# Performance work log

Measured on AMD Instinct MI355X. Metric: run time of the kernel, lower is better.

## Reference

```python
import jax, jax.numpy as jnp
import numpy as np
from jax import lax

N_C = 1024  # number of FPS centroids (hard-coded in forward)
K = 32      # knn neighbors (hard-coded in forward)


def _fps(x, far0):
    # Faithful to the source: dist is recomputed against ONLY the latest
    # centroid each iteration (the mask/min-update in the source is dead code),
    # then far = argmax(dist).
    B = x.shape[0]
    bidx = jnp.arange(B)

    def step(far, _):
        c = x[bidx, far]                              # [B, C]
        d = jnp.sum((x - c[:, None, :]) ** 2, -1)     # [B, N]
        return jnp.argmax(d, -1), c

    _, cents = lax.scan(step, far0, None, length=N_C)  # cents: [n_c, B, C]
    return jnp.transpose(cents, (1, 0, 2))             # [B, n_c, C]


def _knn_group(x, cent):
    # squared euclidean distances (same argsort order as torch.cdist)
    d2 = (jnp.sum(cent ** 2, -1)[..., None]
          + jnp.sum(x ** 2, -1)[:, None, :]
          - 2.0 * jnp.einsum('bmc,bnc->bmn', cent, x))   # [B, n_c, N]
    _, idx = lax.top_k(-d2, K)                            # [B, n_c, K] smallest dists
    neighbors = jax.vmap(lambda xb, ib: xb[ib])(x, idx)   # [B, n_c, K, C]
    return neighbors


def _conv1x1(h, w, b):
    # 1x1 Conv1d == channel matmul; h: [B, Cin, L], w: [Cout, Cin]
    return jax.nn.relu(jnp.einsum('oi,bil->bol', w, h) + b[None, :, None])


def setup_inputs() -> dict:
    key = jax.random.key(0)
    ks = jax.random.split(key, 20)
    B, N, C = 4, 16384, 3
    num_classes = 3
    p = lambda k, shp: (jax.random.normal(k, shp, jnp.float32) * 0.02)
    return {
        'x': jax.random.normal(ks[0], (B, N, C), jnp.float32),
        'far_init': jax.random.randint(ks[1], (B,), 0, N, jnp.int32),
        'w1': p(ks[2], (64, 3)),    'b1': p(ks[3], (64,)),
        'w2': p(ks[4], (64, 64)),   'b2': p(ks[5], (64,)),
        'w3': p(ks[6], (64, 64)),   'b3': p(ks[7], (64,)),
        'w4': p(ks[8], (128, 64)),  'b4': p(ks[9], (128,)),
        'w5': p(ks[10], (1024, 128)), 'b5': p(ks[11], (1024,)),
        'fw1': p(ks[12], (512, 1024)), 'fb1': p(ks[13], (512,)),
        'fw2': p(ks[14], (256, 512)),  'fb2': p(ks[15], (256,)),
        'fw3': p(ks[16], (num_classes, 256)), 'fb3': p(ks[17], (num_classes,)),
    }


def reference(x, far_init, w1, b1, w2, b2, w3, b3, w4, b4, w5, b5,
              fw1, fb1, fw2, fb2, fw3, fb3):
    B, N, C = x.shape
    cent = _fps(x, far_init)                 # [B, n_c, C]
    neighbors = _knn_group(x, cent)          # [B, n_c, K, C]
    h = jnp.transpose(neighbors, (0, 3, 1, 2)).reshape(B, C, N_C * K)
    h = _conv1x1(h, w1, b1)
    h = _conv1x1(h, w2, b2)
    h = _conv1x1(h, w3, b3)
    h = _conv1x1(h, w4, b4)
    h = _conv1x1(h, w5, b5)                  # [B, 1024, n_c*K]
    g = jnp.max(h, axis=2)                   # global max pool -> [B, 1024]
    g = jax.nn.relu(g @ fw1.T + fb1)
    g = jax.nn.relu(g @ fw2.T + fb2)
    return g @ fw3.T + fb3                   # [B, num_classes]
```

## Files before the change

kernel.cpp:

```cpp
#include <hip/hip_runtime.h>

#define BN  4
#define NPT 16384
#define NCC 1024
#define KNN 32

#define HBINS    2048
#define CCH      4
#define CAND_CAP 768

#define OFF_CCOUNT 0
#define OFF_SCOUNT 64
#define OFF_SBITS  128
#define OFF_POOL   (128 + BN*(NPT/32)*4)
#define OFF_CLIST  (OFF_POOL + BN*NCC*4)
#define OFF_H1     (OFF_CLIST + BN*NCC*4)
#define OFF_SLIST  (OFF_H1 + BN*512*4)

typedef short bf16x8 __attribute__((ext_vector_type(8)));
typedef float f32x4  __attribute__((ext_vector_type(4)));
typedef float f32x2  __attribute__((ext_vector_type(2)));

__device__ __forceinline__ short f2bf(float f) {
    unsigned u = __float_as_uint(f);
    return (short)((u + 0x7fffu + ((u >> 16) & 1u)) >> 16);
}
__device__ __forceinline__ bf16x8 cvt8(const float* __restrict__ p) {
    bf16x8 v;
#pragma unroll
    for (int j = 0; j < 8; ++j) v[j] = f2bf(p[j]);
    return v;
}

__global__ __launch_bounds__(512) void fps_kernel(const float* __restrict__ x,
    const int* __restrict__ far_init, int* __restrict__ clist, int* __restrict__ ccount,
    int* __restrict__ scount, unsigned* __restrict__ sbits, float* __restrict__ pool)
{
#pragma clang fp contract(off)
    const int b = blockIdx.x, t = threadIdx.x;
    __shared__ __align__(16) unsigned char seen[NPT];
    __shared__ unsigned long long slot[3];

    sbits[b*(NPT/32) + t] = 0u;
    pool[b*NCC + t] = 0.0f;
    pool[b*NCC + 512 + t] = 0.0f;
    if (t == 0) { ccount[b] = 0; scount[b] = 0; }

    const float* xb = x + (size_t)b * NPT * 3;
    f32x2 px[16], py[16], pz[16];
#pragma unroll
    for (int q = 0; q < 16; ++q) {
        int ia = t + (q << 10), ib = ia + 512;
        px[q] = f32x2{xb[ia*3+0], xb[ib*3+0]};
        py[q] = f32x2{xb[ia*3+1], xb[ib*3+1]};
        pz[q] = f32x2{xb[ia*3+2], xb[ib*3+2]};
    }
    ((uint4*)seen)[t]       = make_uint4(0,0,0,0);
    ((uint4*)seen)[t + 512] = make_uint4(0,0,0,0);
    if (t == 0) { slot[0] = 0ull; slot[1] = 0ull; slot[2] = 0ull; }
    int prev_bx = far_init[b];
    __syncthreads();
    int pbs = __builtin_amdgcn_readfirstlane(prev_bx);
    float cx = xb[pbs*3], cy = xb[pbs*3+1], cz = xb[pbs*3+2];

    int done = 0;
    for (int it = 0; it < NCC-1; ++it) {
        const int p = it % 3;
        const f32x2 cX = {cx, cx}, cY = {cy, cy}, cZ = {cz, cz};
        float best = -1.0f; int bi = 0;
#pragma unroll
        for (int q = 0; q < 16; ++q) {
            f32x2 dx = px[q] - cX;
            f32x2 dy = py[q] - cY;
            f32x2 dz = pz[q] - cZ;
            f32x2 m1 = dx * dx;
            f32x2 m2 = dy * dy;
            f32x2 m3 = dz * dz;
            f32x2 s  = (m1 + m2) + m3;
            int ia = t + (q << 10);
            if (s.x > best) { best = s.x; bi = ia; }
            if (s.y > best) { best = s.y; bi = ia + 512; }
        }
#pragma unroll
        for (int m = 1; m < 64; m <<= 1) {
            float od = __shfl_xor(best, m, 64);
            int   oi = __shfl_xor(bi,   m, 64);
            if (od > best || (od == best && oi < bi)) { best = od; bi = oi; }
        }
        if ((t & 63) == 0) {
            unsigned long long pk =
                (((unsigned long long)__float_as_uint(best)) << 32)
                | (unsigned)(NPT - 1 - bi);
            atomicMax(&slot[p], pk);
        }
        if (t == 0) seen[prev_bx] = 1;
        __syncthreads();
        int bx = NPT - 1 - (int)(unsigned)(slot[p] & 0xFFFFFFFFull);
        if (t == 0) slot[(it + 2) % 3] = 0ull;
        if (seen[bx]) { done = 1; break; }
        prev_bx = bx;
        int bxs = __builtin_amdgcn_readfirstlane(bx);
        cx = xb[bxs*3]; cy = xb[bxs*3+1]; cz = xb[bxs*3+2];
    }
    if (!done && t == 0) seen[prev_bx] = 1;
    __syncthreads();
#pragma unroll
    for (int j = 0; j < 32; ++j) {
        int idx = t + (j << 9);
        if (seen[idx]) {
            int pos = atomicAdd(&ccount[b], 1);
            clist[b * NCC + pos] = idx;
        }
    }
}

__device__ __forceinline__ unsigned key_of(float px, float py, float pz, float xn,
                                           float cx, float cy, float cz, float cn)
{
    float dot = __fadd_rn(__fadd_rn(__fmul_rn(cx,px), __fmul_rn(cy,py)), __fmul_rn(cz,pz));
    float d2  = __fsub_rn(__fadd_rn(cn, xn), __fmul_rn(2.0f, dot));
    unsigned u = __float_as_uint(d2);
    return u ^ ((u >> 31) ? 0xFFFFFFFFu : 0x80000000u);
}

__device__ __forceinline__ void wave_scan_bins(const unsigned* __restrict__ H,
    int nbins, int rem, int lane, int* __restrict__ out_bin, int* __restrict__ out_below)
{
    int per = nbins >> 6;
    int base = lane * per;
    unsigned part = 0;
    for (int q = 0; q < per; ++q) part += H[base + q];
    unsigned inc = part;
#pragma unroll
    for (int m = 1; m < 64; m <<= 1) {
        unsigned u = __shfl_up(inc, m, 64);
        if (lane >= m) inc += u;
    }
    unsigned exc = inc - part;
    unsigned long long mk = __ballot(exc < (unsigned)rem && inc >= (unsigned)rem);
    int src = __ffsll((long long)mk) - 1;
    if (lane == src) {
        unsigned run = exc; int bb = base;
        for (int q = 0; q < per; ++q) {
            unsigned h = H[base + q];
            if (run + h >= (unsigned)rem) { bb = base + q; break; }
            run += h;
        }
        *out_bin = bb; *out_below = (int)run;
    }
}

__global__ __launch_bounds__(1024) void knn_kernel(const float* __restrict__ x,
    const int* __restrict__ clist, const int* __restrict__ ccount,
    unsigned* __restrict__ sbits, int* __restrict__ slist, int* __restrict__ scount)
{
    const int b = blockIdx.y, t = threadIdx.x;
    const int lane = t & 63, w = t >> 6;
    const int cnt = ccount[b];
    const int cbase = blockIdx.x * CCH;
    if (cbase >= cnt) return;
    const float* xb = x + (size_t)b * NPT * 3;

    __shared__ unsigned hist[CCH * HBINS];
    __shared__ unsigned cand[CCH * CAND_CAP];
    __shared__ float cpx[CCH], cpy[CCH], cpz[CCH], cpn[CCH];
    __shared__ unsigned candCnt[CCH];
    __shared__ int s_bb[CCH], s_below[CCH], s_rrem[CCH], s_need[CCH], s_pref[CCH];
    __shared__ unsigned s_tau[CCH];
    __shared__ int s_tbin, s_tbelow;

    if (t < CCH) {
        int ci = clist[b * NCC + min(cbase + t, cnt - 1)];
        float cx = xb[ci*3], cy = xb[ci*3+1], cz = xb[ci*3+2];
        cpx[t] = cx; cpy[t] = cy; cpz[t] = cz;
        cpn[t] = __fadd_rn(__fadd_rn(__fmul_rn(cx,cx), __fmul_rn(cy,cy)), __fmul_rn(cz,cz));
        candCnt[t] = 0;
    }
    for (int i = t; i < CCH * HBINS; i += 1024) hist[i] = 0;
    __syncthreads();

    for (int j = 0; j < NPT/1024; ++j) {
        int i = t + (j << 10);
        float px = xb[i*3], py = xb[i*3+1], pz = xb[i*3+2];
        float xn = __fadd_rn(__fadd_rn(__fmul_rn(px,px), __fmul_rn(py,py)), __fmul_rn(pz,pz));
#pragma unroll
        for (int c = 0; c < CCH; ++c) {
            unsigned key = key_of(px,py,pz,xn, cpx[c],cpy[c],cpz[c],cpn[c]);
            atomicAdd(&hist[c*HBINS + (key >> 21)], 1u);
        }
    }
    __syncthreads();

    if (w < CCH)
        wave_scan_bins(&hist[w*HBINS], HBINS, KNN, lane, &s_bb[w], &s_below[w]);
    __syncthreads();
    if (t < CCH) s_rrem[t] = KNN - s_below[t];
    __syncthreads();

    for (int j = 0; j < NPT/1024; ++j) {
        int i = t + (j << 10);
        float px = xb[i*3], py = xb[i*3+1], pz = xb[i*3+2];
        float xn = __fadd_rn(__fadd_rn(__fmul_rn(px,px), __fmul_rn(py,py)), __fmul_rn(pz,pz));
#pragma unroll
        for (int c = 0; c < CCH; ++c) {
            unsigned key = key_of(px,py,pz,xn, cpx[c],cpy[c],cpz[c],cpn[c]);
            if ((int)(key >> 21) == s_bb[c]) {
                unsigned pos = atomicAdd(&candCnt[c], 1u);
                if (pos < CAND_CAP) cand[c*CAND_CAP + pos] = key;
            }
        }
    }
    __syncthreads();

    if (w < CCH) {
        unsigned cc = candCnt[w];
        if (cc <= CAND_CAP) {
            int r = s_rrem[w] - 1;
            const unsigned* C = &cand[w*CAND_CAP];
            for (int idx = lane; idx < (int)cc; idx += 64) {
                unsigned k = C[idx]; int rank = 0;
                for (int q = 0; q < (int)cc; ++q) {
                    unsigned kq = C[q];
                    rank += (kq < k || (kq == k && q < idx)) ? 1 : 0;
                }
                if (rank == r) s_tau[w] = k;
            }
            if (lane == 0) s_need[w] = 0;
        } else if (lane == 0) s_need[w] = 1;
    }
    __syncthreads();

    for (int c = 0; c < CCH; ++c) {
        if (s_need[c]) {
            const float cx = cpx[c], cy = cpy[c], cz = cpz[c], cn = cpn[c];
            for (int i = t; i < HBINS; i += 1024) hist[i] = 0;
            __syncthreads();
            for (int j = 0; j < NPT/1024; ++j) {
                int i = t + (j << 10);
                float px = xb[i*3], py = xb[i*3+1], pz = xb[i*3+2];
                float xn = __fadd_rn(__fadd_rn(__fmul_rn(px,px), __fmul_rn(py,py)), __fmul_rn(pz,pz));
                unsigned key = key_of(px,py,pz,xn, cx,cy,cz,cn);
                if ((int)(key >> 21) == s_bb[c]) atomicAdd(&hist[(key >> 10) & 2047u], 1u);
            }
            __syncthreads();
            if (w == 0) wave_scan_bins(hist, HBINS, s_rrem[c], lane, &s_tbin, &s_tbelow);
            __syncthreads();
            if (t == 0) { s_pref[c] = (s_bb[c] << 11) | s_tbin; s_rrem[c] -= s_tbelow; }
            __syncthreads();
            for (int i = t; i < 1024; i += 1024) hist[i] = 0;
            __syncthreads();
            for (int j = 0; j < NPT/1024; ++j) {
                int i = t + (j << 10);
                float px = xb[i*3], py = xb[i*3+1], pz = xb[i*3+2];
                float xn = __fadd_rn(__fadd_rn(__fmul_rn(px,px), __fmul_rn(py,py)), __fmul_rn(pz,pz));
                unsigned key = key_of(px,py,pz,xn, cx,cy,cz,cn);
                if ((int)(key >> 10) == s_pref[c]) atomicAdd(&hist[key & 1023u], 1u);
            }
            __syncthreads();
            if (w == 0) wave_scan_bins(hist, 1024, s_rrem[c], lane, &s_tbin, &s_tbelow);
            __syncthreads();
            if (t == 0) s_tau[c] = (((unsigned)s_pref[c]) << 10) | (unsigned)s_tbin;
            __syncthreads();
        }
    }
    __syncthreads();

    for (int j = 0; j < NPT/1024; ++j) {
        int i = t + (j << 10);
        float px = xb[i*3], py = xb[i*3+1], pz = xb[i*3+2];
        float xn = __fadd_rn(__fadd_rn(__fmul_rn(px,px), __fmul_rn(py,py)), __fmul_rn(pz,pz));
        bool sel = false;
#pragma unroll
        for (int c = 0; c < CCH; ++c) {
            unsigned key = key_of(px,py,pz,xn, cpx[c],cpy[c],cpz[c],cpn[c]);
            sel |= (key <= s_tau[c]);
        }
        if (sel) {
            unsigned bit = 1u << (i & 31);
            unsigned old = atomicOr(&sbits[b*(NPT/32) + (i >> 5)], bit);
            if (!(old & bit)) {
                int pos = atomicAdd(&scount[b], 1);
                slist[b * NPT + pos] = i;
            }
        }
    }
}

#define MFMA16(a, bfr, c) __builtin_amdgcn_mfma_f32_16x16x32_bf16(a, bfr, c, 0, 0, 0)

__global__ __launch_bounds__(1024) void mlp_kernel(const float* __restrict__ x,
    const int* __restrict__ sel_list, const int* __restrict__ sel_count,
    const float* __restrict__ w1, const float* __restrict__ b1,
    const float* __restrict__ w2, const float* __restrict__ b2,
    const float* __restrict__ w3, const float* __restrict__ b3,
    const float* __restrict__ w4, const float* __restrict__ b4,
    const float* __restrict__ w5, const float* __restrict__ b5,
    float* __restrict__ pool)
{
    const int b = blockIdx.y, z = blockIdx.z, t = threadIdx.x;
    const int cnt = sel_count[b];
    if ((blockIdx.x << 6) >= cnt) return;
    const int lane = t & 63;
    const int w    = __builtin_amdgcn_readfirstlane(t >> 6);
    const int m    = lane & 15, quad = lane >> 4;

    __shared__ __align__(16) short A1[64 * 72];
    __shared__ __align__(16) short A2[64 * 72];
    __shared__ __align__(16) short A3[64 * 136];
    __shared__ float sx[3 * 64];

    const int ocA = (w >> 2) * 16 + m;
    bf16x8 bw2[2], bw3[2], bw4[2][2], bw5[4];
#pragma unroll
    for (int ks = 0; ks < 2; ++ks) {
        bw2[ks] = cvt8(w2 + ocA*64 + ks*32 + quad*8);
        bw3[ks] = cvt8(w3 + ocA*64 + ks*32 + quad*8);
    }
    int oc4i[2];
#pragma unroll
    for (int r2 = 0; r2 < 2; ++r2) {
        oc4i[r2] = ((w >> 2) + 4*r2) * 16 + m;
#pragma unroll
        for (int ks = 0; ks < 2; ++ks)
            bw4[r2][ks] = cvt8(w4 + oc4i[r2]*64 + ks*32 + quad*8);
    }
    const int oc5 = z*256 + w*16 + m;
#pragma unroll
    for (int ks = 0; ks < 4; ++ks)
        bw5[ks] = cvt8(w5 + oc5*128 + ks*32 + quad*8);
    const float bias2 = b2[ocA], bias3 = b3[ocA];
    const float bias4_0 = b4[oc4i[0]], bias4_1 = b4[oc4i[1]];
    const float bias5 = b5[oc5];
    float w1v[4][3], b1v[4];
#pragma unroll
    for (int i = 0; i < 4; ++i) {
        int oc = w*4 + i;
        w1v[i][0] = w1[oc*3+0]; w1v[i][1] = w1[oc*3+1]; w1v[i][2] = w1[oc*3+2];
        b1v[i] = b1[oc];
    }
    const int pt0 = (w & 3) * 16;

    for (int base = blockIdx.x << 6; base < cnt; base += (32 << 6)) {
        const int npts = min(64, cnt - base);
        __syncthreads();
        if (t < 64) {
            int idx = sel_list[b * NPT + base + min(t, npts - 1)];
            const float* xp = x + ((size_t)b * NPT + idx) * 3;
            sx[t] = xp[0]; sx[64 + t] = xp[1]; sx[128 + t] = xp[2];
        }
        __syncthreads();
        {
            float x0 = sx[lane], x1 = sx[64 + lane], x2 = sx[128 + lane];
#pragma unroll
            for (int i = 0; i < 4; ++i) {
                float acc = fmaf(x2, w1v[i][2], fmaf(x1, w1v[i][1],
                             fmaf(x0, w1v[i][0], b1v[i])));
                A1[lane*72 + w*4 + i] = f2bf(fmaxf(acc, 0.0f));
            }
        }
        __syncthreads();
        {
            bf16x8 a0 = *(const bf16x8*)&A1[(pt0 + m)*72 + quad*8];
            bf16x8 a1 = *(const bf16x8*)&A1[(pt0 + m)*72 + 32 + quad*8];
            f32x4 d = {0.f, 0.f, 0.f, 0.f};
            d = MFMA16(a0, bw2[0], d);
            d = MFMA16(a1, bw2[1], d);
#pragma unroll
            for (int r = 0; r < 4; ++r)
                A2[(pt0 + quad*4 + r)*72 + ocA] = f2bf(fmaxf(d[r] + bias2, 0.0f));
        }
        __syncthreads();
        {
            bf16x8 a0 = *(const bf16x8*)&A2[(pt0 + m)*72 + quad*8];
            bf16x8 a1 = *(const bf16x8*)&A2[(pt0 + m)*72 + 32 + quad*8];
            f32x4 d = {0.f, 0.f, 0.f, 0.f};
            d = MFMA16(a0, bw3[0], d);
            d = MFMA16(a1, bw3[1], d);
#pragma unroll
            for (int r = 0; r < 4; ++r)
                A1[(pt0 + quad*4 + r)*72 + ocA] = f2bf(fmaxf(d[r] + bias3, 0.0f));
        }
        __syncthreads();
        {
            bf16x8 a0 = *(const bf16x8*)&A1[(pt0 + m)*72 + quad*8];
            bf16x8 a1 = *(const bf16x8*)&A1[(pt0 + m)*72 + 32 + quad*8];
#pragma unroll
            for (int r2 = 0; r2 < 2; ++r2) {
                f32x4 d = {0.f, 0.f, 0.f, 0.f};
                d = MFMA16(a0, bw4[r2][0], d);
                d = MFMA16(a1, bw4[r2][1], d);
                float bs = r2 ? bias4_1 : bias4_0;
#pragma unroll
                for (int r = 0; r < 4; ++r)
                    A3[(pt0 + quad*4 + r)*136 + oc4i[r2]] = f2bf(fmaxf(d[r] + bs, 0.0f));
            }
        }
        __syncthreads();
        {
            float vm = 0.0f;
#pragma unroll
            for (int pt4 = 0; pt4 < 4; ++pt4) {
                const int q0 = pt4 * 16;
                f32x4 d = {0.f, 0.f, 0.f, 0.f};
#pragma unroll
                for (int ks = 0; ks < 4; ++ks) {
                    bf16x8 a = *(const bf16x8*)&A3[(q0 + m)*136 + ks*32 + quad*8];
                    d = MFMA16(a, bw5[ks], d);
                }
#pragma unroll
                for (int r = 0; r < 4; ++r)
                    vm = fmaxf(vm, fmaxf(d[r] + bias5, 0.0f));
            }
            vm = fmaxf(vm, __shfl_xor(vm, 16, 64));
            vm = fmaxf(vm, __shfl_xor(vm, 32, 64));
            if (lane < 16)
                atomicMax((int*)&pool[b*NCC + z*256 + w*16 + lane], __float_as_int(vm));
        }
    }
}

__global__ __launch_bounds__(1024) void head1_kernel(const float* __restrict__ pool,
    const float* __restrict__ fw1, const float* __restrict__ fb1,
    float* __restrict__ h1g)
{
    const int bo = blockIdx.x, b = blockIdx.y, t = threadIdx.x;
    const int lane = t & 63, w = t >> 6;
    __shared__ float g[1024];
    g[t] = pool[b*NCC + t];
    __syncthreads();
    int o = bo * 128 + w * 8;
#pragma unroll
    for (int i = 0; i < 8; ++i, ++o) {
        float acc = 0.0f;
#pragma unroll
        for (int j = 0; j < 16; ++j) {
            int k = lane + (j << 6);
            acc += g[k] * fw1[o*1024 + k];
        }
#pragma unroll
        for (int m = 1; m < 64; m <<= 1) acc += __shfl_xor(acc, m, 64);
        if (lane == 0) h1g[b*512 + o] = fmaxf(acc + fb1[o], 0.0f);
    }
}

__global__ __launch_bounds__(1024) void head2_kernel(const float* __restrict__ h1g,
    const float* __restrict__ fw2, const float* __restrict__ fb2,
    const float* __restrict__ fw3, const float* __restrict__ fb3,
    float* __restrict__ out)
{
    const int b = blockIdx.x, t = threadIdx.x;
    const int lane = t & 63, w = t >> 6;
    __shared__ float h1[512], h2[256];
    if (t < 512) h1[t] = h1g[b*512 + t];
    __syncthreads();
#pragma unroll
    for (int i = 0; i < 16; ++i) {
        int o = w * 16 + i;
        float acc = 0.0f;
#pragma unroll
        for (int j = 0; j < 8; ++j) {
            int k = lane + (j << 6);
            acc += h1[k] * fw2[o*512 + k];
        }
#pragma unroll
        for (int m = 1; m < 64; m <<= 1) acc += __shfl_xor(acc, m, 64);
        if (lane == 0) h2[o] = fmaxf(acc + fb2[o], 0.0f);
    }
    __syncthreads();
    if (w < 3) {
        float acc = 0.0f;
#pragma unroll
        for (int j = 0; j < 4; ++j) {
            int k = lane + (j << 6);
            acc += h2[k] * fw3[w*256 + k];
        }
#pragma unroll
        for (int m = 1; m < 64; m <<= 1) acc += __shfl_xor(acc, m, 64);
        if (lane == 0) out[b*3 + w] = acc + fb3[w];
    }
}

extern "C" void kernel_launch(void* const* d_in, const int* in_sizes, int n_in,
                              void* d_out, int out_size, void* d_ws, size_t ws_size,
                              hipStream_t stream)
{
    const float* x    = (const float*)d_in[0];
    const int*   far0 = (const int*)  d_in[1];
    const float *w1 = (const float*)d_in[2],  *b1 = (const float*)d_in[3];
    const float *w2 = (const float*)d_in[4],  *b2 = (const float*)d_in[5];
    const float *w3 = (const float*)d_in[6],  *b3 = (const float*)d_in[7];
    const float *w4 = (const float*)d_in[8],  *b4 = (const float*)d_in[9];
    const float *w5 = (const float*)d_in[10], *b5 = (const float*)d_in[11];
    const float *fw1 = (const float*)d_in[12], *fb1 = (const float*)d_in[13];
    const float *fw2 = (const float*)d_in[14], *fb2 = (const float*)d_in[15];
    const float *fw3 = (const float*)d_in[16], *fb3 = (const float*)d_in[17];

    char* ws = (char*)d_ws;
    int*      ccount = (int*)     (ws + OFF_CCOUNT);
    int*      scount = (int*)     (ws + OFF_SCOUNT);
    unsigned* sbits  = (unsigned*)(ws + OFF_SBITS);
    float*    pool   = (float*)   (ws + OFF_POOL);
    int*      clist  = (int*)     (ws + OFF_CLIST);
    float*    h1g    = (float*)   (ws + OFF_H1);
    int*      slist  = (int*)     (ws + OFF_SLIST);

    fps_kernel<<<BN, 512, 0, stream>>>(x, far0, clist, ccount, scount, sbits, pool);
    knn_kernel<<<dim3(NCC/CCH, BN), 1024, 0, stream>>>(x, clist, ccount, sbits, slist, scount);
    mlp_kernel<<<dim3(32, BN, 4), 1024, 0, stream>>>(x, slist, scount,
        w1,b1, w2,b2, w3,b3, w4,b4, w5,b5, pool);
    head1_kernel<<<dim3(4, BN), 1024, 0, stream>>>(pool, fw1, fb1, h1g);
    head2_kernel<<<BN, 1024, 0, stream>>>(h1g, fw2,fb2, fw3,fb3, (float*)d_out);
}
```

Before: 194.7 us.

## Widen FPS block, cache kNN keys in registers, fuse head kernels, halve centroid chunk

The FPS kernel now runs 1024 threads per batch, so each thread holds 16 points instead of 32 and the serial per-iteration distance/argmax loop is shorter. The kNN kernel keeps computed distance keys in registers instead of recomputing them in the candidate and selection passes. It also processes 2 centroids per block instead of 4, giving more blocks. The two head kernels are fused into one, removing a launch and a global round trip. Risks are higher register pressure in kNN, more cross-wave reduction and atomics in FPS, and each kNN block rescanning the point cloud for fewer centroids.

```diff
diff --git a/kernel.cpp b/kernel.cpp
--- a/kernel.cpp
+++ b/kernel.cpp
@@ -6,7 +6,7 @@
 #define KNN 32
 
 #define HBINS    2048
-#define CCH      4
+#define CCH      2
 #define CAND_CAP 768
 
 #define OFF_CCOUNT 0
@@ -14,8 +14,7 @@
 #define OFF_SBITS  128
 #define OFF_POOL   (128 + BN*(NPT/32)*4)
 #define OFF_CLIST  (OFF_POOL + BN*NCC*4)
-#define OFF_H1     (OFF_CLIST + BN*NCC*4)
-#define OFF_SLIST  (OFF_H1 + BN*512*4)
+#define OFF_SLIST  (OFF_CLIST + BN*NCC*4)
 
 typedef short bf16x8 __attribute__((ext_vector_type(8)));
 typedef float f32x4  __attribute__((ext_vector_type(4)));
@@ -32,7 +31,7 @@
     return v;
 }
 
-__global__ __launch_bounds__(512) void fps_kernel(const float* __restrict__ x,
+__global__ __launch_bounds__(1024) void fps_kernel(const float* __restrict__ x,
     const int* __restrict__ far_init, int* __restrict__ clist, int* __restrict__ ccount,
     int* __restrict__ scount, unsigned* __restrict__ sbits, float* __restrict__ pool)
 {
@@ -41,22 +40,20 @@
     __shared__ __align__(16) unsigned char seen[NPT];
     __shared__ unsigned long long slot[3];
 
-    sbits[b*(NPT/32) + t] = 0u;
+    if (t < 512) sbits[b*(NPT/32) + t] = 0u;
     pool[b*NCC + t] = 0.0f;
-    pool[b*NCC + 512 + t] = 0.0f;
     if (t == 0) { ccount[b] = 0; scount[b] = 0; }
 
     const float* xb = x + (size_t)b * NPT * 3;
-    f32x2 px[16], py[16], pz[16];
-#pragma unroll
-    for (int q = 0; q < 16; ++q) {
-        int ia = t + (q << 10), ib = ia + 512;
-        px[q] = f32x2{xb[ia*3+0], xb[ib*3+0]};
-        py[q] = f32x2{xb[ia*3+1], xb[ib*3+1]};
-        pz[q] = f32x2{xb[ia*3+2], xb[ib*3+2]};
-    }
-    ((uint4*)seen)[t]       = make_uint4(0,0,0,0);
-    ((uint4*)seen)[t + 512] = make_uint4(0,0,0,0);
+    f32x2 px[8], py[8], pz[8];
+#pragma unroll
+    for (int r = 0; r < 8; ++r) {
+        int ia = t + ((2*r) << 10), ib = ia + 1024;
+        px[r] = f32x2{xb[ia*3+0], xb[ib*3+0]};
+        py[r] = f32x2{xb[ia*3+1], xb[ib*3+1]};
+        pz[r] = f32x2{xb[ia*3+2], xb[ib*3+2]};
+    }
+    ((uint4*)seen)[t] = make_uint4(0,0,0,0);
     if (t == 0) { slot[0] = 0ull; slot[1] = 0ull; slot[2] = 0ull; }
     int prev_bx = far_init[b];
     __syncthreads();
@@ -69,17 +66,17 @@
         const f32x2 cX = {cx, cx}, cY = {cy, cy}, cZ = {cz, cz};
         float best = -1.0f; int bi = 0;
 #pragma unroll
-        for (int q = 0; q < 16; ++q) {
-            f32x2 dx = px[q] - cX;
-            f32x2 dy = py[q] - cY;
-            f32x2 dz = pz[q] - cZ;
+        for (int r = 0; r < 8; ++r) {
+            f32x2 dx = px[r] - cX;
+            f32x2 dy = py[r] - cY;
+            f32x2 dz = pz[r] - cZ;
             f32x2 m1 = dx * dx;
             f32x2 m2 = dy * dy;
             f32x2 m3 = dz * dz;
             f32x2 s  = (m1 + m2) + m3;
-            int ia = t + (q << 10);
+            int ia = t + ((2*r) << 10);
             if (s.x > best) { best = s.x; bi = ia; }
-            if (s.y > best) { best = s.y; bi = ia + 512; }
+            if (s.y > best) { best = s.y; bi = ia + 1024; }
         }
 #pragma unroll
         for (int m = 1; m < 64; m <<= 1) {
@@ -105,8 +102,8 @@
     if (!done && t == 0) seen[prev_bx] = 1;
     __syncthreads();
 #pragma unroll
-    for (int j = 0; j < 32; ++j) {
-        int idx = t + (j << 9);
+    for (int j = 0; j < 16; ++j) {
+        int idx = t + (j << 10);
         if (seen[idx]) {
             int pos = atomicAdd(&ccount[b], 1);
             clist[b * NCC + pos] = idx;
@@ -179,6 +176,8 @@
     for (int i = t; i < CCH * HBINS; i += 1024) hist[i] = 0;
     __syncthreads();
 
+    unsigned keys[NPT/1024][CCH];
+#pragma unroll
     for (int j = 0; j < NPT/1024; ++j) {
         int i = t + (j << 10);
         float px = xb[i*3], py = xb[i*3+1], pz = xb[i*3+2];
@@ -186,6 +185,7 @@
 #pragma unroll
         for (int c = 0; c < CCH; ++c) {
             unsigned key = key_of(px,py,pz,xn, cpx[c],cpy[c],cpz[c],cpn[c]);
+            keys[j][c] = key;
             atomicAdd(&hist[c*HBINS + (key >> 21)], 1u);
         }
     }
@@ -197,13 +197,11 @@
     if (t < CCH) s_rrem[t] = KNN - s_below[t];
     __syncthreads();
 
+#pragma unroll
     for (int j = 0; j < NPT/1024; ++j) {
-        int i = t + (j << 10);
-        float px = xb[i*3], py = xb[i*3+1], pz = xb[i*3+2];
-        float xn = __fadd_rn(__fadd_rn(__fmul_rn(px,px), __fmul_rn(py,py)), __fmul_rn(pz,pz));
 #pragma unroll
         for (int c = 0; c < CCH; ++c) {
-            unsigned key = key_of(px,py,pz,xn, cpx[c],cpy[c],cpz[c],cpn[c]);
+            unsigned key = keys[j][c];
             if ((int)(key >> 21) == s_bb[c]) {
                 unsigned pos = atomicAdd(&candCnt[c], 1u);
                 if (pos < CAND_CAP) cand[c*CAND_CAP + pos] = key;
@@ -265,16 +263,12 @@
     }
     __syncthreads();
 
+#pragma unroll
     for (int j = 0; j < NPT/1024; ++j) {
         int i = t + (j << 10);
-        float px = xb[i*3], py = xb[i*3+1], pz = xb[i*3+2];
-        float xn = __fadd_rn(__fadd_rn(__fmul_rn(px,px), __fmul_rn(py,py)), __fmul_rn(pz,pz));
         bool sel = false;
 #pragma unroll
-        for (int c = 0; c < CCH; ++c) {
-            unsigned key = key_of(px,py,pz,xn, cpx[c],cpy[c],cpz[c],cpn[c]);
-            sel |= (key <= s_tau[c]);
-        }
+        for (int c = 0; c < CCH; ++c) sel |= (keys[j][c] <= s_tau[c]);
         if (sel) {
             unsigned bit = 1u << (i & 31);
             unsigned old = atomicOr(&sbits[b*(NPT/32) + (i >> 5)], bit);
@@ -419,18 +413,21 @@
     }
 }
 
-__global__ __launch_bounds__(1024) void head1_kernel(const float* __restrict__ pool,
+__global__ __launch_bounds__(1024) void head_kernel(const float* __restrict__ pool,
     const float* __restrict__ fw1, const float* __restrict__ fb1,
-    float* __restrict__ h1g)
-{
-    const int bo = blockIdx.x, b = blockIdx.y, t = threadIdx.x;
-    const int lane = t & 63, w = t >> 6;
-    __shared__ float g[1024];
+    const float* __restrict__ fw2, const float* __restrict__ fb2,
+    const float* __restrict__ fw3, const float* __restrict__ fb3,
+    float* __restrict__ out)
+{
+    const int b = blockIdx.x, t = threadIdx.x;
+    const int lane = t & 63;
+    const int w = __builtin_amdgcn_readfirstlane(t >> 6);
+    __shared__ float g[1024], h1[512], h2[256];
     g[t] = pool[b*NCC + t];
     __syncthreads();
-    int o = bo * 128 + w * 8;
-#pragma unroll
-    for (int i = 0; i < 8; ++i, ++o) {
+#pragma unroll
+    for (int i = 0; i < 32; ++i) {
+        int o = w * 32 + i;
         float acc = 0.0f;
 #pragma unroll
         for (int j = 0; j < 16; ++j) {
@@ -439,19 +436,8 @@
         }
 #pragma unroll
         for (int m = 1; m < 64; m <<= 1) acc += __shfl_xor(acc, m, 64);
-        if (lane == 0) h1g[b*512 + o] = fmaxf(acc + fb1[o], 0.0f);
-    }
-}
-
-__global__ __launch_bounds__(1024) void head2_kernel(const float* __restrict__ h1g,
-    const float* __restrict__ fw2, const float* __restrict__ fb2,
-    const float* __restrict__ fw3, const float* __restrict__ fb3,
-    float* __restrict__ out)
-{
-    const int b = blockIdx.x, t = threadIdx.x;
-    const int lane = t & 63, w = t >> 6;
-    __shared__ float h1[512], h2[256];
-    if (t < 512) h1[t] = h1g[b*512 + t];
+        if (lane == 0) h1[o] = fmaxf(acc + fb1[o], 0.0f);
+    }
     __syncthreads();
 #pragma unroll
     for (int i = 0; i < 16; ++i) {
@@ -501,13 +487,11 @@
     unsigned* sbits  = (unsigned*)(ws + OFF_SBITS);
     float*    pool   = (float*)   (ws + OFF_POOL);
     int*      clist  = (int*)     (ws + OFF_CLIST);
-    float*    h1g    = (float*)   (ws + OFF_H1);
     int*      slist  = (int*)     (ws + OFF_SLIST);
 
-    fps_kernel<<<BN, 512, 0, stream>>>(x, far0, clist, ccount, scount, sbits, pool);
+    fps_kernel<<<BN, 1024, 0, stream>>>(x, far0, clist, ccount, scount, sbits, pool);
     knn_kernel<<<dim3(NCC/CCH, BN), 1024, 0, stream>>>(x, clist, ccount, sbits, slist, scount);
     mlp_kernel<<<dim3(32, BN, 4), 1024, 0, stream>>>(x, slist, scount,
         w1,b1, w2,b2, w3,b3, w4,b4, w5,b5, pool);
-    head1_kernel<<<dim3(4, BN), 1024, 0, stream>>>(pool, fw1, fb1, h1g);
-    head2_kernel<<<BN, 1024, 0, stream>>>(h1g, fw2,fb2, fw3,fb3, (float*)d_out);
-}
+    head_kernel<<<BN, 1024, 0, stream>>>(pool, fw1,fb1, fw2,fb2, fw3,fb3, (float*)d_out);
+}
```

Result: faster. 184.9 us (-5.0%).
